# Optimization experiments

Hardware: AMD Instinct MI355X
Metric: run time of the kernel (lower is better)

Reference implementation:

```python
import jax, jax.numpy as jnp
import numpy as np

NEG_SLOPE = 0.2
EPS = 1e-16


def _gat_conv(x, src, dst, edge_attr, W, We, att_src, att_dst, att_edge, bias):
    """PyG GATConv, heads=H, concat=False, edge_dim given. x:[N,F_in]."""
    N = x.shape[0]
    H, C = att_src.shape
    xs = (x @ W.T).reshape(N, H, C)                      # [N,H,C]
    a_src = jnp.einsum('nhc,hc->nh', xs, att_src)        # [N,H]
    a_dst = jnp.einsum('nhc,hc->nh', xs, att_dst)        # [N,H]
    e = (edge_attr @ We.T).reshape(-1, H, C)             # [E,H,C]
    a_edge = jnp.einsum('ehc,hc->eh', e, att_edge)       # [E,H]
    alpha = a_src[src] + a_dst[dst] + a_edge             # [E,H]
    alpha = jax.nn.leaky_relu(alpha, NEG_SLOPE)
    # segment softmax over destination nodes (per head)
    amax = jax.ops.segment_max(alpha, dst, num_segments=N)   # [N,H]
    ex = jnp.exp(alpha - amax[dst])
    denom = jax.ops.segment_sum(ex, dst, num_segments=N)     # [N,H]
    alpha = ex / (denom[dst] + EPS)
    msg = xs[src] * alpha[..., None]                     # [E,H,C]
    out = jax.ops.segment_sum(msg, dst, num_segments=N)  # [N,H,C]
    return out.mean(axis=1) + bias                       # concat=False -> mean over heads


def _add_self_loops(src, dst, edge_attr, N):
    # PyG add_self_loops with fill_value='mean': per-dst mean of incoming edge_attr
    ones = jnp.ones((edge_attr.shape[0],), edge_attr.dtype)
    sums = jax.ops.segment_sum(edge_attr, dst, num_segments=N)
    cnt = jax.ops.segment_sum(ones, dst, num_segments=N)
    loop_attr = sums / jnp.maximum(cnt, 1.0)[:, None]
    idx = jnp.arange(N, dtype=src.dtype)
    return (jnp.concatenate([src, idx]), jnp.concatenate([dst, idx]),
            jnp.concatenate([edge_attr, loop_attr], axis=0))


def setup_inputs() -> dict:
    key = jax.random.key(0)
    ks = jax.random.split(key, 16)
    N, E, F_IN, C, H = 100000, 1600000, 64, 32, 4
    s = 0.1
    inp = {
        'x': jax.random.normal(ks[0], (N, F_IN), jnp.float32),
        'edge_index': jax.random.randint(ks[1], (2, E), 0, N, jnp.int32),
        'edge_weight': jax.random.uniform(ks[2], (E, 1), jnp.float32),
        'w1': jax.random.normal(ks[3], (H * C, F_IN), jnp.float32) * s,
        'we1': jax.random.normal(ks[4], (H * C, 1), jnp.float32) * s,
        'as1': jax.random.normal(ks[5], (H, C), jnp.float32) * s,
        'ad1': jax.random.normal(ks[6], (H, C), jnp.float32) * s,
        'ae1': jax.random.normal(ks[7], (H, C), jnp.float32) * s,
        'b1': jnp.zeros((C,), jnp.float32),
        'w2': jax.random.normal(ks[8], (H * C, C), jnp.float32) * s,
        'we2': jax.random.normal(ks[9], (H * C, 1), jnp.float32) * s,
        'as2': jax.random.normal(ks[10], (H, C), jnp.float32) * s,
        'ad2': jax.random.normal(ks[11], (H, C), jnp.float32) * s,
        'ae2': jax.random.normal(ks[12], (H, C), jnp.float32) * s,
        'b2': jnp.zeros((C,), jnp.float32),
    }
    return inp


def reference(x, edge_index, edge_weight, w1, we1, as1, ad1, ae1, b1,
              w2, we2, as2, ad2, ae2, b2):
    N = x.shape[0]
    src, dst, ea = _add_self_loops(edge_index[0], edge_index[1], edge_weight, N)
    h = jax.nn.relu(_gat_conv(x, src, dst, ea, w1, we1, as1, ad1, ae1, b1))
    # nn.Dropout is identity in eval mode
    h = jax.nn.relu(_gat_conv(h, src, dst, ea, w2, we2, as2, ad2, ae2, b2))
    return h
```

## Files before the change

kernel.cpp:

```cpp
#include <hip/hip_runtime.h>
#include <hip/hip_fp16.h>
#include <cstddef>

#define GAT_EPS 1e-16f
#define SCAN_BS 256

__global__ void k_scanA(const unsigned long long* __restrict__ pk,
                        float* __restrict__ loopat, int* __restrict__ cnt,
                        int* __restrict__ incl, int* __restrict__ bsum, int N) {
    __shared__ int sh[SCAN_BS];
    int i = blockIdx.x * SCAN_BS + threadIdx.x;
    int cv = 0;
    if (i < N) {
        unsigned long long v = pk[i];
        cv = (int)(v >> 44);
        float sum = (float)(v & ((1ULL << 44) - 1)) * (1.0f / 16777216.0f);
        loopat[i] = sum / fmaxf((float)cv, 1.0f);
        cnt[i] = cv;
    }
    int v = (i < N) ? cv + 1 : 0;
    sh[threadIdx.x] = v;
    __syncthreads();
    for (int off = 1; off < SCAN_BS; off <<= 1) {
        int t = (threadIdx.x >= off) ? sh[threadIdx.x - off] : 0;
        __syncthreads();
        sh[threadIdx.x] += t;
        __syncthreads();
    }
    if (i < N) incl[i] = sh[threadIdx.x];
    if (threadIdx.x == SCAN_BS - 1) bsum[blockIdx.x] = sh[threadIdx.x];
}

__global__ void k_scanB(int* __restrict__ bsum, int nb,
                        const float* __restrict__ we1, const float* __restrict__ ae1,
                        const float* __restrict__ we2, const float* __restrict__ ae2,
                        float* __restrict__ wd) {
    int t = threadIdx.x;
    if (t < 128) {
        float v1 = we1[t] * ae1[t];
        float v2 = we2[t] * ae2[t];
#pragma unroll
        for (int off = 16; off; off >>= 1) {
            v1 += __shfl_xor(v1, off);
            v2 += __shfl_xor(v2, off);
        }
        if ((t & 31) == 0) { wd[t >> 5] = v1; wd[4 + (t >> 5)] = v2; }
    }
    __shared__ int sh[512];
    int v = (t < nb) ? bsum[t] : 0;
    sh[t] = v;
    __syncthreads();
    for (int off = 1; off < 512; off <<= 1) {
        int u = (t >= off) ? sh[t - off] : 0;
        __syncthreads();
        sh[t] += u;
        __syncthreads();
    }
    if (t < nb) bsum[t] = sh[t] - v;
}

__global__ void k_scanC(const int* __restrict__ cnt, const int* __restrict__ incl,
                        const int* __restrict__ bsum, int* __restrict__ rowptr,
                        int N, int Etot) {
    int i = blockIdx.x * SCAN_BS + threadIdx.x;
    if (i < N) rowptr[i] = bsum[blockIdx.x] + incl[i] - (cnt[i] + 1);
    if (i == N - 1) rowptr[N] = Etot;
}

__global__ void k_scatter(const int* __restrict__ src, const int* __restrict__ dst,
                          const float* __restrict__ ew, const float* __restrict__ loopat,
                          const int* __restrict__ cnt, const int* __restrict__ pos,
                          const int* __restrict__ rowptr, int2* __restrict__ epk,
                          int E, int Etot) {
    int e = blockIdx.x * blockDim.x + threadIdx.x;
    if (e >= Etot) return;
    int s, d, p; float ea;
    if (e < E) { s = src[e]; d = dst[e]; ea = ew[e]; p = pos[e]; }
    else       { s = e - E; d = s;       ea = loopat[s]; p = cnt[d]; }
    int2 q; q.x = s; q.y = __float_as_int(ea);
    epk[rowptr[d] + p] = q;
}

__global__ __launch_bounds__(256, 2)
void k_gemm1h(const float* __restrict__ x, const float* __restrict__ W,
              const float* __restrict__ as_, const float* __restrict__ ad_,
              __half* __restrict__ xs, float* __restrict__ asrc,
              float* __restrict__ adst, int N, int gemmb,
              const int* __restrict__ dst, const float* __restrict__ ew,
              unsigned long long* __restrict__ pk, int* __restrict__ pos, int E) {
    int g = blockIdx.x / 5;
    int r = blockIdx.x % 5;
    if (r != 0) {
        int i = (g * 4 + r - 1) * 256 + threadIdx.x;
        if (i < E) {
            int d = dst[i];
            unsigned long long add = (1ULL << 44) |
                (unsigned long long)(ew[i] * 16777216.0f + 0.5f);
            unsigned long long old = atomicAdd(&pk[d], add);
            pos[i] = (int)(old >> 44);
        }
        return;
    }
    if (g >= gemmb) return;

    int n0 = g * 64;
    int t = threadIdx.x;
    int tx = t & 31;
    int ty = t >> 5;
    __shared__ __half Wh[64 * 132];
    __shared__ float xsh[64 * 65];
    int nrows = min(64, N - n0);
    for (int j = t; j < 8192; j += 256) {
        int c = j >> 6, k = j & 63;
        Wh[k * 132 + ((c & 31) << 2) + (c >> 5)] = __float2half(W[j]);
    }
    const float* xg = x + (size_t)n0 * 64;
    for (int j = t; j < nrows * 64; j += 256) xsh[(j >> 6) * 65 + (j & 63)] = xg[j];
    __syncthreads();

    float acc[8][4];
#pragma unroll
    for (int i = 0; i < 8; i++)
#pragma unroll
        for (int j = 0; j < 4; j++) acc[i][j] = 0.f;

#pragma unroll 4
    for (int k = 0; k < 64; k++) {
        const __half2* wp = reinterpret_cast<const __half2*>(&Wh[k * 132 + (tx << 2)]);
        float2 wf0 = __half22float2(wp[0]);
        float2 wf1 = __half22float2(wp[1]);
#pragma unroll
        for (int i = 0; i < 8; i++) {
            float xv = xsh[(ty * 8 + i) * 65 + k];
            acc[i][0] += xv * wf0.x;
            acc[i][1] += xv * wf0.y;
            acc[i][2] += xv * wf1.x;
            acc[i][3] += xv * wf1.y;
        }
    }

    float asv[4], adv[4];
#pragma unroll
    for (int j = 0; j < 4; j++) { asv[j] = as_[32 * j + tx]; adv[j] = ad_[32 * j + tx]; }

#pragma unroll
    for (int i = 0; i < 8; i++) {
        int row = ty * 8 + i;
        bool ok = row < nrows;
        __half* orow = xs + (size_t)(n0 + row) * 128;
#pragma unroll
        for (int j = 0; j < 4; j++) {
            if (ok) orow[32 * j + tx] = __float2half(acc[i][j]);
            float vs = acc[i][j] * asv[j];
            float vd = acc[i][j] * adv[j];
#pragma unroll
            for (int off = 16; off; off >>= 1) {
                vs += __shfl_xor(vs, off);
                vd += __shfl_xor(vd, off);
            }
            if (ok && tx == 0) {
                asrc[(size_t)(n0 + row) * 4 + j] = vs;
                adst[(size_t)(n0 + row) * 4 + j] = vd;
            }
        }
    }
}

__global__ __launch_bounds__(256, 2)
void k_gemm2(const float* __restrict__ h1, const float* __restrict__ W2,
             const float* __restrict__ as_, const float* __restrict__ ad_,
             __half* __restrict__ xs, float* __restrict__ asrc,
             float* __restrict__ adst, int N) {
    int n0 = blockIdx.x * 64;
    int t = threadIdx.x;
    int tx = t & 31;
    int ty = t >> 5;
    __shared__ __half Wh[32 * 132];
    __shared__ float xsh[64 * 33];
    int nrows = min(64, N - n0);
    for (int j = t; j < 4096; j += 256) {
        int c = j >> 5, k = j & 31;
        Wh[k * 132 + ((c & 31) << 2) + (c >> 5)] = __float2half(W2[j]);
    }
    const float* xg = h1 + (size_t)n0 * 32;
    for (int j = t; j < nrows * 32; j += 256) xsh[(j >> 5) * 33 + (j & 31)] = xg[j];
    __syncthreads();

    float acc[8][4];
#pragma unroll
    for (int i = 0; i < 8; i++)
#pragma unroll
        for (int j = 0; j < 4; j++) acc[i][j] = 0.f;

#pragma unroll 4
    for (int k = 0; k < 32; k++) {
        const __half2* wp = reinterpret_cast<const __half2*>(&Wh[k * 132 + (tx << 2)]);
        float2 wf0 = __half22float2(wp[0]);
        float2 wf1 = __half22float2(wp[1]);
#pragma unroll
        for (int i = 0; i < 8; i++) {
            float xv = xsh[(ty * 8 + i) * 33 + k];
            acc[i][0] += xv * wf0.x;
            acc[i][1] += xv * wf0.y;
            acc[i][2] += xv * wf1.x;
            acc[i][3] += xv * wf1.y;
        }
    }

    float asv[4], adv[4];
#pragma unroll
    for (int j = 0; j < 4; j++) { asv[j] = as_[32 * j + tx]; adv[j] = ad_[32 * j + tx]; }

#pragma unroll
    for (int i = 0; i < 8; i++) {
        int row = ty * 8 + i;
        bool ok = row < nrows;
        __half* orow = xs + (size_t)(n0 + row) * 128;
#pragma unroll
        for (int j = 0; j < 4; j++) {
            if (ok) orow[32 * j + tx] = __float2half(acc[i][j]);
            float vs = acc[i][j] * asv[j];
            float vd = acc[i][j] * adv[j];
#pragma unroll
            for (int off = 16; off; off >>= 1) {
                vs += __shfl_xor(vs, off);
                vd += __shfl_xor(vd, off);
            }
            if (ok && tx == 0) {
                asrc[(size_t)(n0 + row) * 4 + j] = vs;
                adst[(size_t)(n0 + row) * 4 + j] = vd;
            }
        }
    }
}

__global__ void k_gather(const int2* __restrict__ epk, const int* __restrict__ rowptr,
                         const __half* __restrict__ xs,
                         const float* __restrict__ asrc, const float* __restrict__ adst,
                         const float* __restrict__ wedot, const float* __restrict__ bias,
                         float* __restrict__ out, int N) {
    int node = blockIdx.x * 4 + (threadIdx.x >> 6);
    if (node >= N) return;
    int l = threadIdx.x & 63;
    int q = l >> 4;
    int p = l & 15;
    int h = p >> 2;
    float wd = wedot[h];
    float ad = adst[(size_t)node * 4 + h];
    int beg = rowptr[node], end = rowptr[node + 1];

    float a0 = 0.f, a1 = 0.f, a2 = 0.f, a3 = 0.f;
    float a4 = 0.f, a5 = 0.f, a6 = 0.f, a7 = 0.f, ds = 0.f;
#pragma unroll 2
    for (int i = beg; i < end; i += 4) {
        int idx = i + q;
        bool valid = idx < end;
        int2 e = epk[valid ? idx : end - 1];
        int s = e.x;
        float as = asrc[(size_t)s * 4 + h];
        float al = as + ad + __int_as_float(e.y) * wd;
        al = fmaxf(al, 0.2f * al);
        float w = valid ? __expf(al) : 0.f;
        uint4 raw = reinterpret_cast<const uint4*>(xs + (size_t)s * 128)[p];
        const __half2* hp = reinterpret_cast<const __half2*>(&raw);
        float2 f0 = __half22float2(hp[0]);
        float2 f1 = __half22float2(hp[1]);
        float2 f2 = __half22float2(hp[2]);
        float2 f3 = __half22float2(hp[3]);
        a0 += w * f0.x; a1 += w * f0.y;
        a2 += w * f1.x; a3 += w * f1.y;
        a4 += w * f2.x; a5 += w * f2.y;
        a6 += w * f3.x; a7 += w * f3.y;
        ds += w;
    }
    a0 += __shfl_xor(a0, 16); a1 += __shfl_xor(a1, 16);
    a2 += __shfl_xor(a2, 16); a3 += __shfl_xor(a3, 16);
    a4 += __shfl_xor(a4, 16); a5 += __shfl_xor(a5, 16);
    a6 += __shfl_xor(a6, 16); a7 += __shfl_xor(a7, 16);
    ds += __shfl_xor(ds, 16);
    a0 += __shfl_xor(a0, 32); a1 += __shfl_xor(a1, 32);
    a2 += __shfl_xor(a2, 32); a3 += __shfl_xor(a3, 32);
    a4 += __shfl_xor(a4, 32); a5 += __shfl_xor(a5, 32);
    a6 += __shfl_xor(a6, 32); a7 += __shfl_xor(a7, 32);
    ds += __shfl_xor(ds, 32);
    float inv = 1.f / (ds + GAT_EPS);
    a0 *= inv; a1 *= inv; a2 *= inv; a3 *= inv;
    a4 *= inv; a5 *= inv; a6 *= inv; a7 *= inv;
    a0 += __shfl_xor(a0, 4); a1 += __shfl_xor(a1, 4);
    a2 += __shfl_xor(a2, 4); a3 += __shfl_xor(a3, 4);
    a4 += __shfl_xor(a4, 4); a5 += __shfl_xor(a5, 4);
    a6 += __shfl_xor(a6, 4); a7 += __shfl_xor(a7, 4);
    a0 += __shfl_xor(a0, 8); a1 += __shfl_xor(a1, 8);
    a2 += __shfl_xor(a2, 8); a3 += __shfl_xor(a3, 8);
    a4 += __shfl_xor(a4, 8); a5 += __shfl_xor(a5, 8);
    a6 += __shfl_xor(a6, 8); a7 += __shfl_xor(a7, 8);
    if (l < 4) {
        int c0 = l * 8;
        float4 r0, r1;
        r0.x = fmaxf(0.25f * a0 + bias[c0 + 0], 0.f);
        r0.y = fmaxf(0.25f * a1 + bias[c0 + 1], 0.f);
        r0.z = fmaxf(0.25f * a2 + bias[c0 + 2], 0.f);
        r0.w = fmaxf(0.25f * a3 + bias[c0 + 3], 0.f);
        r1.x = fmaxf(0.25f * a4 + bias[c0 + 4], 0.f);
        r1.y = fmaxf(0.25f * a5 + bias[c0 + 5], 0.f);
        r1.z = fmaxf(0.25f * a6 + bias[c0 + 6], 0.f);
        r1.w = fmaxf(0.25f * a7 + bias[c0 + 7], 0.f);
        float4* op = reinterpret_cast<float4*>(out + (size_t)node * 32 + c0);
        op[0] = r0;
        op[1] = r1;
    }
}

extern "C" void kernel_launch(void* const* d_in, const int* in_sizes, int n_in,
                              void* d_out, int out_size, void* d_ws, size_t ws_size,
                              hipStream_t stream) {
    const float* x   = (const float*)d_in[0];
    const int*   ei  = (const int*)d_in[1];
    const float* ewt = (const float*)d_in[2];
    const float* w1  = (const float*)d_in[3];
    const float* we1 = (const float*)d_in[4];
    const float* as1 = (const float*)d_in[5];
    const float* ad1 = (const float*)d_in[6];
    const float* ae1 = (const float*)d_in[7];
    const float* b1  = (const float*)d_in[8];
    const float* w2  = (const float*)d_in[9];
    const float* we2 = (const float*)d_in[10];
    const float* as2 = (const float*)d_in[11];
    const float* ad2 = (const float*)d_in[12];
    const float* ae2 = (const float*)d_in[13];
    const float* b2  = (const float*)d_in[14];

    const int N = in_sizes[0] / 64;
    const int E = in_sizes[1] / 2;
    const int Etot = E + N;
    const int* srcI = ei;
    const int* dstI = ei + E;
    const int nb = (N + SCAN_BS - 1) / SCAN_BS;

    char* base = (char*)d_ws;
    size_t off = 0;
    auto alloc = [&](size_t bytes) { char* p = base + off; off += (bytes + 15) & ~(size_t)15; return p; };
    __half* xs    = (__half*)alloc((size_t)N * 128 * sizeof(__half));
    float* h1     = (float*)alloc((size_t)N * 32 * sizeof(float));
    float* asrc   = (float*)alloc((size_t)N * 4 * sizeof(float));
    float* adst   = (float*)alloc((size_t)N * 4 * sizeof(float));
    float* loopat = (float*)alloc((size_t)N * sizeof(float));
    unsigned long long* pk = (unsigned long long*)alloc((size_t)N * sizeof(unsigned long long));
    int*   cnt    = (int*)alloc((size_t)N * sizeof(int));
    int*   incl   = (int*)alloc((size_t)N * sizeof(int));
    int*   bsum   = (int*)alloc(512 * sizeof(int));
    int*   rowptr = (int*)alloc((size_t)(N + 1) * sizeof(int));
    int*   pos    = (int*)alloc((size_t)E * sizeof(int));
    int2*  epk    = (int2*)alloc((size_t)Etot * sizeof(int2));
    float* wedot  = (float*)alloc(8 * sizeof(float));

    float* outF = (float*)d_out;

    hipMemsetAsync(pk, 0, (size_t)N * sizeof(unsigned long long), stream);

    const int gemmb = (N + 63) / 64;
    const int histb = (E + 255) / 256;
    const int G = gemmb > (histb + 3) / 4 ? gemmb : (histb + 3) / 4;
    const int gb = (N + 3) / 4;

    k_gemm1h<<<5 * G, 256, 0, stream>>>(x, w1, as1, ad1, xs, asrc, adst, N, gemmb,
                                        dstI, ewt, pk, pos, E);

    k_scanA<<<nb, SCAN_BS, 0, stream>>>(pk, loopat, cnt, incl, bsum, N);
    k_scanB<<<1, 512, 0, stream>>>(bsum, nb, we1, ae1, we2, ae2, wedot);
    k_scanC<<<nb, SCAN_BS, 0, stream>>>(cnt, incl, bsum, rowptr, N, Etot);
    k_scatter<<<(Etot + 255) / 256, 256, 0, stream>>>(srcI, dstI, ewt, loopat,
                                                      cnt, pos, rowptr, epk, E, Etot);

    k_gather<<<gb, 256, 0, stream>>>(epk, rowptr, xs, asrc, adst,
                                     wedot + 0, b1, h1, N);

    k_gemm2<<<gemmb, 256, 0, stream>>>(h1, w2, as2, ad2, xs, asrc, adst, N);
    k_gather<<<gb, 256, 0, stream>>>(epk, rowptr, xs, asrc, adst,
                                     wedot + 4, b2, outF, N);
}
```

Measured before the change: 322.2 us.

## Handle self-loops inside gather and drop rowptr scan pass

Self-loop edges are no longer materialised in the CSR edge list. The gather kernel recomputes the mean incoming edge attribute from the edges it already reads and adds the self-loop term directly. The 64-bit packed atomic histogram becomes a 32-bit count atomic, and the separate rowptr kernel is removed by computing row start from bsum+incl-cnt on the fly. This removes one launch, the loopat buffer and N scatter writes. In exchange it adds extra index arithmetic and a self-loop xs load per node in each gather, and a per-node attribute reduction.

```diff
diff --git a/kernel.cpp b/kernel.cpp
--- a/kernel.cpp
+++ b/kernel.cpp
@@ -5,20 +5,11 @@
 #define GAT_EPS 1e-16f
 #define SCAN_BS 256
 
-__global__ void k_scanA(const unsigned long long* __restrict__ pk,
-                        float* __restrict__ loopat, int* __restrict__ cnt,
-                        int* __restrict__ incl, int* __restrict__ bsum, int N) {
+__global__ void k_scanA(const int* __restrict__ cnt, int* __restrict__ incl,
+                        int* __restrict__ bsum, int N) {
     __shared__ int sh[SCAN_BS];
     int i = blockIdx.x * SCAN_BS + threadIdx.x;
-    int cv = 0;
-    if (i < N) {
-        unsigned long long v = pk[i];
-        cv = (int)(v >> 44);
-        float sum = (float)(v & ((1ULL << 44) - 1)) * (1.0f / 16777216.0f);
-        loopat[i] = sum / fmaxf((float)cv, 1.0f);
-        cnt[i] = cv;
-    }
-    int v = (i < N) ? cv + 1 : 0;
+    int v = (i < N) ? cnt[i] : 0;
     sh[threadIdx.x] = v;
     __syncthreads();
     for (int off = 1; off < SCAN_BS; off <<= 1) {
@@ -59,26 +50,16 @@
     if (t < nb) bsum[t] = sh[t] - v;
 }
 
-__global__ void k_scanC(const int* __restrict__ cnt, const int* __restrict__ incl,
-                        const int* __restrict__ bsum, int* __restrict__ rowptr,
-                        int N, int Etot) {
-    int i = blockIdx.x * SCAN_BS + threadIdx.x;
-    if (i < N) rowptr[i] = bsum[blockIdx.x] + incl[i] - (cnt[i] + 1);
-    if (i == N - 1) rowptr[N] = Etot;
-}
-
 __global__ void k_scatter(const int* __restrict__ src, const int* __restrict__ dst,
-                          const float* __restrict__ ew, const float* __restrict__ loopat,
-                          const int* __restrict__ cnt, const int* __restrict__ pos,
-                          const int* __restrict__ rowptr, int2* __restrict__ epk,
-                          int E, int Etot) {
+                          const float* __restrict__ ew, const int* __restrict__ pos,
+                          const int* __restrict__ incl, const int* __restrict__ cnt,
+                          const int* __restrict__ bsum, int2* __restrict__ epk, int E) {
     int e = blockIdx.x * blockDim.x + threadIdx.x;
-    if (e >= Etot) return;
-    int s, d, p; float ea;
-    if (e < E) { s = src[e]; d = dst[e]; ea = ew[e]; p = pos[e]; }
-    else       { s = e - E; d = s;       ea = loopat[s]; p = cnt[d]; }
-    int2 q; q.x = s; q.y = __float_as_int(ea);
-    epk[rowptr[d] + p] = q;
+    if (e >= E) return;
+    int d = dst[e];
+    int base = bsum[d >> 8] + incl[d] - cnt[d];
+    int2 q; q.x = src[e]; q.y = __float_as_int(ew[e]);
+    epk[base + pos[e]] = q;
 }
 
 __global__ __launch_bounds__(256, 2)
@@ -86,18 +67,15 @@
               const float* __restrict__ as_, const float* __restrict__ ad_,
               __half* __restrict__ xs, float* __restrict__ asrc,
               float* __restrict__ adst, int N, int gemmb,
-              const int* __restrict__ dst, const float* __restrict__ ew,
-              unsigned long long* __restrict__ pk, int* __restrict__ pos, int E) {
+              const int* __restrict__ dst, int* __restrict__ cnt,
+              int* __restrict__ pos, int E) {
     int g = blockIdx.x / 5;
     int r = blockIdx.x % 5;
     if (r != 0) {
         int i = (g * 4 + r - 1) * 256 + threadIdx.x;
         if (i < E) {
             int d = dst[i];
-            unsigned long long add = (1ULL << 44) |
-                (unsigned long long)(ew[i] * 16777216.0f + 0.5f);
-            unsigned long long old = atomicAdd(&pk[d], add);
-            pos[i] = (int)(old >> 44);
+            pos[i] = atomicAdd(&cnt[d], 1);
         }
         return;
     }
@@ -234,7 +212,8 @@
     }
 }
 
-__global__ void k_gather(const int2* __restrict__ epk, const int* __restrict__ rowptr,
+__global__ void k_gather(const int2* __restrict__ epk, const int* __restrict__ incl,
+                         const int* __restrict__ cnt, const int* __restrict__ bsum,
                          const __half* __restrict__ xs,
                          const float* __restrict__ asrc, const float* __restrict__ adst,
                          const float* __restrict__ wedot, const float* __restrict__ bias,
@@ -247,16 +226,20 @@
     int h = p >> 2;
     float wd = wedot[h];
     float ad = adst[(size_t)node * 4 + h];
-    int beg = rowptr[node], end = rowptr[node + 1];
+    int cv = cnt[node];
+    int beg = bsum[node >> 8] + incl[node] - cv;
+    int end = beg + cv;
 
     float a0 = 0.f, a1 = 0.f, a2 = 0.f, a3 = 0.f;
-    float a4 = 0.f, a5 = 0.f, a6 = 0.f, a7 = 0.f, ds = 0.f;
+    float a4 = 0.f, a5 = 0.f, a6 = 0.f, a7 = 0.f, ds = 0.f, easum = 0.f;
 #pragma unroll 2
     for (int i = beg; i < end; i += 4) {
         int idx = i + q;
         bool valid = idx < end;
         int2 e = epk[valid ? idx : end - 1];
         int s = e.x;
+        float eav = valid ? __int_as_float(e.y) : 0.f;
+        easum += eav;
         float as = asrc[(size_t)s * 4 + h];
         float al = as + ad + __int_as_float(e.y) * wd;
         al = fmaxf(al, 0.2f * al);
@@ -272,6 +255,25 @@
         a4 += w * f2.x; a5 += w * f2.y;
         a6 += w * f3.x; a7 += w * f3.y;
         ds += w;
+    }
+    easum += __shfl_xor(easum, 16);
+    easum += __shfl_xor(easum, 32);
+    float loop_ea = easum / fmaxf((float)cv, 1.0f);
+    float aln = asrc[(size_t)node * 4 + h] + ad + loop_ea * wd;
+    aln = fmaxf(aln, 0.2f * aln);
+    float wl = __expf(aln);
+    if (q == 0) {
+        uint4 raw = reinterpret_cast<const uint4*>(xs + (size_t)node * 128)[p];
+        const __half2* hp = reinterpret_cast<const __half2*>(&raw);
+        float2 f0 = __half22float2(hp[0]);
+        float2 f1 = __half22float2(hp[1]);
+        float2 f2 = __half22float2(hp[2]);
+        float2 f3 = __half22float2(hp[3]);
+        a0 += wl * f0.x; a1 += wl * f0.y;
+        a2 += wl * f1.x; a3 += wl * f1.y;
+        a4 += wl * f2.x; a5 += wl * f2.y;
+        a6 += wl * f3.x; a7 += wl * f3.y;
+        ds += wl;
     }
     a0 += __shfl_xor(a0, 16); a1 += __shfl_xor(a1, 16);
     a2 += __shfl_xor(a2, 16); a3 += __shfl_xor(a3, 16);
@@ -332,7 +334,6 @@
 
     const int N = in_sizes[0] / 64;
     const int E = in_sizes[1] / 2;
-    const int Etot = E + N;
     const int* srcI = ei;
     const int* dstI = ei + E;
     const int nb = (N + SCAN_BS - 1) / SCAN_BS;
@@ -344,19 +345,16 @@
     float* h1     = (float*)alloc((size_t)N * 32 * sizeof(float));
     float* asrc   = (float*)alloc((size_t)N * 4 * sizeof(float));
     float* adst   = (float*)alloc((size_t)N * 4 * sizeof(float));
-    float* loopat = (float*)alloc((size_t)N * sizeof(float));
-    unsigned long long* pk = (unsigned long long*)alloc((size_t)N * sizeof(unsigned long long));
     int*   cnt    = (int*)alloc((size_t)N * sizeof(int));
     int*   incl   = (int*)alloc((size_t)N * sizeof(int));
     int*   bsum   = (int*)alloc(512 * sizeof(int));
-    int*   rowptr = (int*)alloc((size_t)(N + 1) * sizeof(int));
     int*   pos    = (int*)alloc((size_t)E * sizeof(int));
-    int2*  epk    = (int2*)alloc((size_t)Etot * sizeof(int2));
+    int2*  epk    = (int2*)alloc((size_t)E * sizeof(int2));
     float* wedot  = (float*)alloc(8 * sizeof(float));
 
     float* outF = (float*)d_out;
 
-    hipMemsetAsync(pk, 0, (size_t)N * sizeof(unsigned long long), stream);
+    hipMemsetAsync(cnt, 0, (size_t)N * sizeof(int), stream);
 
     const int gemmb = (N + 63) / 64;
     const int histb = (E + 255) / 256;
@@ -364,18 +362,17 @@
     const int gb = (N + 3) / 4;
 
     k_gemm1h<<<5 * G, 256, 0, stream>>>(x, w1, as1, ad1, xs, asrc, adst, N, gemmb,
-                                        dstI, ewt, pk, pos, E);
-
-    k_scanA<<<nb, SCAN_BS, 0, stream>>>(pk, loopat, cnt, incl, bsum, N);
+                                        dstI, cnt, pos, E);
+
+    k_scanA<<<nb, SCAN_BS, 0, stream>>>(cnt, incl, bsum, N);
     k_scanB<<<1, 512, 0, stream>>>(bsum, nb, we1, ae1, we2, ae2, wedot);
-    k_scanC<<<nb, SCAN_BS, 0, stream>>>(cnt, incl, bsum, rowptr, N, Etot);
-    k_scatter<<<(Etot + 255) / 256, 256, 0, stream>>>(srcI, dstI, ewt, loopat,
-                                                      cnt, pos, rowptr, epk, E, Etot);
-
-    k_gather<<<gb, 256, 0, stream>>>(epk, rowptr, xs, asrc, adst,
+    k_scatter<<<(E + 255) / 256, 256, 0, stream>>>(srcI, dstI, ewt, pos,
+                                                   incl, cnt, bsum, epk, E);
+
+    k_gather<<<gb, 256, 0, stream>>>(epk, incl, cnt, bsum, xs, asrc, adst,
                                      wedot + 0, b1, h1, N);
 
     k_gemm2<<<gemmb, 256, 0, stream>>>(h1, w2, as2, ad2, xs, asrc, adst, N);
-    k_gather<<<gb, 256, 0, stream>>>(epk, rowptr, xs, asrc, adst,
+    k_gather<<<gb, 256, 0, stream>>>(epk, incl, cnt, bsum, xs, asrc, adst,
                                      wedot + 4, b2, outF, N);
 }
```

Result: no change. 323.5 us (+0.4%).
